# Optimization experiments

Hardware: AMD Instinct MI355X
Metric: run time of the kernel (lower is better)

The kernel has to match this reference:

```python
import jax, jax.numpy as jnp
import numpy as np

H = 16          # n_heads
HID = 64        # QASS MLP hidden dim


def setup_inputs() -> dict:
    key = jax.random.key(0)
    ks = jax.random.split(key, 12)
    B, N, D = 2, 2048, 1024
    Dh = D // H
    inp = {
        "query": jax.random.normal(ks[0], (B, N, D), jnp.float32),
        "key": jax.random.normal(ks[1], (B, N, D), jnp.float32),
        "value": jax.random.normal(ks[2], (B, N, D), jnp.float32),
        "allowed_mask": jnp.ones((1, 1, N, N), dtype=bool),
        # projection weights, torch Linear convention: y = x @ W.T, W: [out, in]
        "wq": jax.random.normal(ks[3], (D, D), jnp.float32) * (D ** -0.5),
        "wk": jax.random.normal(ks[4], (D, D), jnp.float32) * (D ** -0.5),
        "wv": jax.random.normal(ks[5], (D, D), jnp.float32) * (D ** -0.5),
        "wo": jax.random.normal(ks[6], (D, D), jnp.float32) * (D ** -0.5),
        # QASS scaler weights
        "wb1": jax.random.normal(ks[7], (HID, 1), jnp.float32),          # mlp_base[0]
        "wb2": jax.random.normal(ks[8], (H * Dh, HID), jnp.float32) * (HID ** -0.5),  # mlp_base[2]
        "wg1": jax.random.normal(ks[9], (HID, Dh), jnp.float32) * (Dh ** -0.5),       # mlp_gate[0]
        "wg2": jax.random.normal(ks[10], (Dh, HID), jnp.float32) * (HID ** -0.5),     # mlp_gate[2]
        "n_context": 2048,
    }
    return inp


def _gelu(x):
    return jax.nn.gelu(x, approximate=False)  # torch nn.GELU default (erf)


def reference(query, key, value, allowed_mask, wq, wk, wv, wo, wb1, wb2, wg1, wg2, n_context):
    B, N, D = query.shape
    Dh = D // H

    def split_heads(x):  # [B,N,D] -> [B,H,N,Dh]
        return x.reshape(B, N, H, Dh).transpose(0, 2, 1, 3)

    q = split_heads(query @ wq.T)
    k = split_heads(key @ wk.T)
    v = split_heads(value @ wv.T)

    # QASS scaling: q * base(log n) * (1 + tanh(gate(q)))   (n_context > 1)
    log_n = jnp.log(jnp.asarray(n_context, jnp.float32))
    base = (_gelu(log_n * wb1[:, 0]) @ wb2.T).reshape(1, H, 1, Dh)  # [1,H,1,Dh]
    gate = 1.0 + jnp.tanh(_gelu(q @ wg1.T) @ wg2.T)                  # [B,H,N,Dh]
    q = q * base * gate

    scores = jnp.einsum("bhnd,bhmd->bhnm", q, k) / jnp.sqrt(jnp.float32(Dh))
    scores = jnp.where(allowed_mask, scores, -jnp.inf)
    attn = jax.nn.softmax(scores, axis=-1)  # dropout p=0 -> identity
    out = jnp.einsum("bhnm,bhmd->bhnd", attn, v)
    out = out.transpose(0, 2, 1, 3).reshape(B, N, D)
    return out @ wo.T
```

## Files before the change

kernel.cpp:

```cpp
#include <hip/hip_runtime.h>
#include <math.h>


typedef _Float16 half_t;
using half8   = __attribute__((ext_vector_type(8))) _Float16;
using bhalf8  = __attribute__((ext_vector_type(8))) short;
using floatx4 = __attribute__((ext_vector_type(4))) float;

__device__ inline unsigned short f2bf(float f) {
  union { float f; unsigned int u; } v; v.f = f;
  unsigned int u = v.u;
  u = u + 0x7fffu + ((u >> 16) & 1u);
  return (unsigned short)(u >> 16);
}
__device__ inline float bf2f(unsigned short h) {
  union { unsigned int u; float f; } v; v.u = ((unsigned int)h) << 16;
  return v.f;
}
__device__ inline float gelu_f(float x) {
  return 0.5f * x * (1.0f + erff(x * 0.70710678118654752440f));
}
__device__ __forceinline__ unsigned int cvtpk_bf16(float lo, float hi) {
  unsigned int r;
  asm("v_cvt_pk_bf16_f32 %0, %1, %2" : "=v"(r) : "v"(lo), "v"(hi));
  return r;
}

#define MFMAF16(a, b, c)  __builtin_amdgcn_mfma_f32_16x16x32_f16((a), (b), (c), 0, 0, 0)
#define MFMABF16(a, b, c) __builtin_amdgcn_mfma_f32_16x16x32_bf16((a), (b), (c), 0, 0, 0)

__device__ __forceinline__ void dma16(const void* g, void* l) {
  __builtin_amdgcn_global_load_lds(
      (const __attribute__((address_space(1))) unsigned int*)g,
      (__attribute__((address_space(3))) unsigned int*)l, 16, 0, 0);
}

__global__ __launch_bounds__(256) void k_cvtbase(
    const float* __restrict__ q, const float* __restrict__ k, const float* __restrict__ v,
    const float* __restrict__ wq, const float* __restrict__ wk,
    const float* __restrict__ wv, const float* __restrict__ wo,
    half_t* __restrict__ q16, half_t* __restrict__ k16, half_t* __restrict__ v16,
    half_t* __restrict__ w16,
    const float* __restrict__ wb1, const float* __restrict__ wb2,
    const int* __restrict__ nctx, float* __restrict__ base_out) {
  int tid = threadIdx.x;
  if (blockIdx.x >= 8192) {
    __shared__ float h1[64];
    float logn = logf((float)(*nctx));
    if (tid < 64) h1[tid] = gelu_f(logn * wb1[tid]);
    __syncthreads();
    int i = (blockIdx.x - 8192) * 256 + tid;
    float s = 0.f;
#pragma unroll
    for (int j = 0; j < 64; j++) s += h1[j] * wb2[i * 64 + j];
    base_out[i] = s;
    return;
  }
  size_t e = ((size_t)blockIdx.x * 256 + tid) * 8;
  const float* src; half_t* dst; size_t off;
  if (e < (size_t)3 * 4194304) {
    int t = (int)(e >> 22); off = e & 4194303;
    src = (t == 0) ? q : (t == 1 ? k : v);
    dst = (t == 0) ? q16 : (t == 1 ? k16 : v16);
  } else {
    size_t e2 = e - (size_t)3 * 4194304;
    int t = (int)(e2 >> 20); off = (e2 & 1048575);
    src = (t == 0) ? wq : (t == 1 ? wk : (t == 2 ? wv : wo));
    dst = w16 + (size_t)t * 1048576;
  }
  float4 a = *(const float4*)(src + off);
  float4 b = *(const float4*)(src + off + 4);
  half8 h;
  h[0] = (half_t)a.x; h[1] = (half_t)a.y; h[2] = (half_t)a.z; h[3] = (half_t)a.w;
  h[4] = (half_t)b.x; h[5] = (half_t)b.y; h[6] = (half_t)b.z; h[7] = (half_t)b.w;
  *(half8*)(dst + off) = h;
}

template <int MODE>
__global__ __launch_bounds__(256, 3) void k_gemm(const half_t* __restrict__ Abase,
                                                 const half_t* __restrict__ Wbase,
                                                 half_t* __restrict__ qp16,
                                                 half_t* __restrict__ kswz,
                                                 unsigned short* __restrict__ vtl,
                                                 float* __restrict__ outf) {
  const int z = (MODE == 0) ? blockIdx.z : 0;
  const half_t* Ag = Abase + (size_t)z * 4194304;
  const half_t* Wg = Wbase + (size_t)z * 1048576;
  __shared__ __align__(16) half_t SM[4][128 * 32];
  const int tid = threadIdx.x, lane = tid & 63, w = tid >> 6;
  const int quad = lane >> 4, lm = lane & 15;
  const int wm = w >> 1, wn = w & 1;
  const int bm0 = blockIdx.y * 128, bn0 = blockIdx.x * 128;

  const floatx4 zero4 = {0.f, 0.f, 0.f, 0.f};
  floatx4 acc[4][4];
#pragma unroll
  for (int i = 0; i < 4; i++)
#pragma unroll
    for (int j = 0; j < 4; j++) acc[i][j] = zero4;

  const int j4 = lane >> 2;
  const int cs = (lane & 3) ^ (((j4 & 3) + (j4 >> 2)) & 3);
  const int ub = ((lm & 3) + (lm >> 2)) & 3;

#pragma unroll
  for (int i = 0; i < 2; i++) {
    int tr = w * 32 + i * 16 + j4;
    dma16((const char*)Ag + ((size_t)(bm0 + tr) * 1024 + cs * 8) * 2,
          (char*)SM[0] + (w * 32 + i * 16) * 64);
    dma16((const char*)Wg + ((size_t)(bn0 + tr) * 1024 + cs * 8) * 2,
          (char*)SM[2] + (w * 32 + i * 16) * 64);
  }

  for (int kk = 0; kk < 1024; kk += 32) {
    const int cur = (kk >> 5) & 1;
    __syncthreads();
    if (kk < 992) {
#pragma unroll
      for (int i = 0; i < 2; i++) {
        int tr = w * 32 + i * 16 + j4;
        dma16((const char*)Ag + ((size_t)(bm0 + tr) * 1024 + kk + 32 + cs * 8) * 2,
              (char*)SM[cur ^ 1] + (w * 32 + i * 16) * 64);
        dma16((const char*)Wg + ((size_t)(bn0 + tr) * 1024 + kk + 32 + cs * 8) * 2,
              (char*)SM[2 + (cur ^ 1)] + (w * 32 + i * 16) * 64);
      }
    }

    const half_t* as_ = SM[cur];
    const half_t* bs_ = SM[2 + cur];
    half8 af[4], bf[4];
#pragma unroll
    for (int tm = 0; tm < 4; tm++)
      af[tm] = *(const half8*)&as_[(wm * 64 + tm * 16 + lm) * 32
                                   + ((quad ^ ub) << 3)];
#pragma unroll
    for (int tn = 0; tn < 4; tn++)
      bf[tn] = *(const half8*)&bs_[(wn * 64 + tn * 16 + lm) * 32
                                   + ((quad ^ ub) << 3)];
#pragma unroll
    for (int tm = 0; tm < 4; tm++)
#pragma unroll
      for (int tn = 0; tn < 4; tn++)
        acc[tm][tn] = MFMAF16(af[tm], bf[tn], acc[tm][tn]);
  }

  if constexpr (MODE == 3) {
#pragma unroll
    for (int tm = 0; tm < 4; tm++)
#pragma unroll
      for (int tn = 0; tn < 4; tn++)
#pragma unroll
        for (int rr = 0; rr < 4; rr++) {
          int gm = bm0 + wm * 64 + tm * 16 + quad * 4 + rr;
          int gn = bn0 + wn * 64 + tn * 16 + lm;
          outf[(size_t)gm * 1024 + gn] = acc[tm][tn][rr];
        }
  } else if (z == 0) {
#pragma unroll
    for (int tm = 0; tm < 4; tm++)
#pragma unroll
      for (int tn = 0; tn < 4; tn++)
#pragma unroll
        for (int rr = 0; rr < 4; rr++) {
          int gm = bm0 + wm * 64 + tm * 16 + quad * 4 + rr;
          int gn = bn0 + wn * 64 + tn * 16 + lm;
          int b = gm >> 11, n = gm & 2047, hd = gn >> 6, d = gn & 63;
          qp16[((size_t)((b << 4) + hd) * 2048 + n) * 64 + d] = (half_t)acc[tm][tn][rr];
        }
  } else if (z == 1) {
    half_t* smh = (half_t*)&SM[0][0];
    __syncthreads();
#pragma unroll
    for (int tm = 0; tm < 4; tm++)
#pragma unroll
      for (int tn = 0; tn < 4; tn++) {
        int gnl = wn * 64 + tn * 16 + lm;
        int hl = gnl >> 6, d = gnl & 63;
#pragma unroll
        for (int rr = 0; rr < 4; rr++) {
          int nl = wm * 64 + tm * 16 + quad * 4 + rr;
          int sw = ((((d >> 3) ^ (nl & 7)) << 3) | (d & 7));
          smh[(hl * 128 + nl) * 64 + sw] = (half_t)acc[tm][tn][rr];
        }
      }
    __syncthreads();
    {
      const int b = bm0 >> 11, n0 = bm0 & 2047, hd0 = bn0 >> 6;
#pragma unroll
      for (int c = 0; c < 8; c++) {
        int lin = (c * 256 + tid) * 8;
        int hl = lin >> 13, nl = (lin >> 6) & 127, j0 = lin & 63;
        size_t row = (size_t)((b << 4) + hd0 + hl) * 2048 + n0 + nl;
        *(half8*)(kswz + row * 64 + j0) = *(const half8*)(smh + lin);
      }
    }
  } else {
    unsigned short* sm = (unsigned short*)&SM[0][0];
    __syncthreads();
#pragma unroll
    for (int tm = 0; tm < 4; tm++) {
      int nlb = wm * 64 + tm * 16 + quad * 4;
      int tl = (nlb >> 6) & 1, nnb = nlb & 63;
      int kc4 = nnb >> 5;
      int qd = (nnb >> 2) & 3;
      int jb = (nnb >> 4) & 1;
#pragma unroll
      for (int tn = 0; tn < 4; tn++) {
        int gnl = wn * 64 + tn * 16 + lm;
        int hl = gnl >> 6, d = gnl & 63;
        int inner0 = (qd * 16 + (d & 15)) * 32 + (d >> 4) * 8 + jb * 4;
        unsigned int u0 = __float_as_uint(acc[tm][tn][0]) + 0x8000u;
        unsigned int u1 = __float_as_uint(acc[tm][tn][1]) + 0x8000u;
        unsigned int u2 = __float_as_uint(acc[tm][tn][2]) + 0x8000u;
        unsigned int u3 = __float_as_uint(acc[tm][tn][3]) + 0x8000u;
        uint2 pk;
        pk.x = __builtin_amdgcn_perm(u1, u0, 0x07060302u);
        pk.y = __builtin_amdgcn_perm(u3, u2, 0x07060302u);
        *(uint2*)&sm[(((hl * 2 + tl) * 2 + kc4) * 2048) + inner0] = pk;
      }
    }
    __syncthreads();
    {
      const int b = bm0 >> 11, t0 = (bm0 & 2047) >> 6, hd0 = bn0 >> 6;
#pragma unroll
      for (int c = 0; c < 8; c++) {
        int lin = (c * 256 + tid) * 8;
        int page = lin >> 11;
        int hl = page >> 2, tl = (page >> 1) & 1, kc4 = page & 1;
        int inner = lin & 2047;
        size_t idx = ((size_t)(((b << 4) + hd0 + hl) * 32 + t0 + tl) * 2 + kc4) * 2048
                   + (size_t)inner;
        *(bhalf8*)(vtl + idx) = *(const bhalf8*)(sm + lin);
      }
    }
  }
}

__global__ __launch_bounds__(256) void k_gate(const half_t* __restrict__ qp,
                                              const float* __restrict__ base_v,
                                              const float* __restrict__ wg1,
                                              const float* __restrict__ wg2,
                                              half_t* __restrict__ qs) {
  __shared__ __align__(16) half_t W1[64 * 72];
  __shared__ __align__(16) half_t W2[64 * 72];
  __shared__ __align__(16) half_t HT[4][16 * 72];
  const int tid = threadIdx.x, lane = tid & 63, w = tid >> 6;
  const int quad = lane >> 4, lm = lane & 15;
  for (int i = tid; i < 4096; i += 256) {
    int j = i >> 6, d = i & 63;
    W1[j * 72 + d] = (half_t)wg1[i];
    W2[j * 72 + d] = (half_t)wg2[i];
  }
  __syncthreads();
  const int R0 = blockIdx.x * 256;
  const int hd = (R0 >> 11) & 15;
  float bsev[4];
#pragma unroll
  for (int tn = 0; tn < 4; tn++) bsev[tn] = base_v[hd * 64 + tn * 16 + lm];
  const float cs = 0.18033688011112042f;
  const floatx4 zero4 = {0.f, 0.f, 0.f, 0.f};
  half_t* ht = HT[w];

  for (int ti = 0; ti < 4; ti++) {
    int r0 = R0 + w * 64 + ti * 16;
    half8 aq0 = *(const half8*)&qp[(size_t)(r0 + lm) * 64 + quad * 8];
    half8 aq1 = *(const half8*)&qp[(size_t)(r0 + lm) * 64 + 32 + quad * 8];
    floatx4 hc[4];
#pragma unroll
    for (int tn = 0; tn < 4; tn++) {
      half8 b0 = *(const half8*)&W1[(tn * 16 + lm) * 72 + quad * 8];
      half8 b1 = *(const half8*)&W1[(tn * 16 + lm) * 72 + 32 + quad * 8];
      floatx4 t = zero4;
      t = MFMAF16(aq0, b0, t);
      t = MFMAF16(aq1, b1, t);
      hc[tn] = t;
    }
#pragma unroll
    for (int tn = 0; tn < 4; tn++)
#pragma unroll
      for (int rr = 0; rr < 4; rr++)
        ht[(quad * 4 + rr) * 72 + tn * 16 + lm] = (half_t)gelu_f(hc[tn][rr]);
    half8 ah0 = *(const half8*)&ht[lm * 72 + quad * 8];
    half8 ah1 = *(const half8*)&ht[lm * 72 + 32 + quad * 8];
#pragma unroll
    for (int tn = 0; tn < 4; tn++) {
      half8 b0 = *(const half8*)&W2[(tn * 16 + lm) * 72 + quad * 8];
      half8 b1 = *(const half8*)&W2[(tn * 16 + lm) * 72 + 32 + quad * 8];
      floatx4 t = zero4;
      t = MFMAF16(ah0, b0, t);
      t = MFMAF16(ah1, b1, t);
#pragma unroll
      for (int rr = 0; rr < 4; rr++) {
        int row = r0 + quad * 4 + rr;
        int d = tn * 16 + lm;
        float qv = (float)qp[(size_t)row * 64 + d];
        float g = 1.0f + tanhf(t[rr]);
        qs[(size_t)row * 64 + d] = (half_t)(qv * bsev[tn] * g * cs);
      }
    }
  }
}

__global__ __launch_bounds__(256, 2) void k_attn(const half_t* __restrict__ qs,
                                                 const half_t* __restrict__ kswz,
                                                 const unsigned short* __restrict__ vtl,
                                                 unsigned short* __restrict__ Opart,
                                                 float* __restrict__ rpart) {
  __shared__ __align__(16) half_t KH[2][64 * 64];

  const int tid = threadIdx.x;
  const int lane = tid & 63;
  const int w = tid >> 6;
  const int quad = lane >> 4;
  const int lm = lane & 15;
  const int a7 = lm & 7;
  const int hd = blockIdx.x;
  const int qg = blockIdx.y >> 1, half = blockIdx.y & 1;
  const int b = blockIdx.z;
  const int bh = b * 16 + hd;
  const size_t hb = (size_t)bh * 2048 * 64;
  const char* khT = (const char*)(kswz + hb);
  const unsigned short* vtT = vtl + (size_t)bh * 32 * 4096;

  half8 qh[4][2];
#pragma unroll
  for (int rg = 0; rg < 4; rg++)
#pragma unroll
    for (int kc = 0; kc < 2; kc++)
      qh[rg][kc] = *(const half8*)(qs + hb
          + (size_t)(qg * 256 + w * 64 + rg * 16 + lm) * 64 + kc * 32 + quad * 8);

  const floatx4 zero4 = {0.f, 0.f, 0.f, 0.f};
  floatx4 O[4][4];
#pragma unroll
  for (int rg = 0; rg < 4; rg++)
#pragma unroll
    for (int dt = 0; dt < 4; dt++) O[rg][dt] = zero4;
  floatx4 racc[4];
#pragma unroll
  for (int rg = 0; rg < 4; rg++) racc[rg] = zero4;
  const short one_bf = (short)0x3F80;
  const bhalf8 vones = {one_bf, one_bf, one_bf, one_bf,
                        one_bf, one_bf, one_bf, one_bf};

  const int lo16 = lane * 16;
  const size_t g0 = (size_t)half * 16 * 8192;

#pragma unroll
  for (int r = 0; r < 2; r++) {
    int sb = (w * 2 + r) * 1024;
    dma16(khT + g0 + sb + lo16, (char*)KH[0] + sb);
  }

  for (int t = 0; t < 16; t++) {
    const int cur = t & 1;
    __syncthreads();

    const unsigned short* vb = vtT + ((size_t)(half * 16 + t) * 2) * 2048 + lane * 32;
    bhalf8 vf[2][4];
#pragma unroll
    for (int kc4 = 0; kc4 < 2; kc4++)
#pragma unroll
      for (int dt = 0; dt < 4; dt++)
        vf[kc4][dt] = *(const bhalf8*)(vb + kc4 * 2048 + dt * 8);

    if (t < 15) {
      const size_t gof = g0 + (size_t)(t + 1) * 8192;
#pragma unroll
      for (int r = 0; r < 2; r++) {
        int sb = (w * 2 + r) * 1024;
        dma16(khT + gof + sb + lo16, (char*)KH[cur ^ 1] + sb);
      }
    }

    const half_t* kh_ = KH[cur];

#pragma unroll
    for (int p = 0; p < 2; p++) {
      floatx4 s[2][4];
#pragma unroll
      for (int ri = 0; ri < 2; ri++)
#pragma unroll
        for (int kb = 0; kb < 4; kb++) s[ri][kb] = zero4;

      __builtin_amdgcn_s_setprio(1);
#pragma unroll
      for (int kb = 0; kb < 4; kb++)
#pragma unroll
        for (int kc = 0; kc < 2; kc++) {
          int addr = (kb * 16 + lm) * 64 + (((kc * 4 + quad) ^ a7) << 3);
          half8 khf = *(const half8*)&kh_[addr];
#pragma unroll
          for (int ri = 0; ri < 2; ri++)
            s[ri][kb] = MFMAF16(khf, qh[p * 2 + ri][kc], s[ri][kb]);
        }
      __builtin_amdgcn_s_setprio(0);

#pragma unroll
      for (int ri = 0; ri < 2; ri++) {
        const int rg = p * 2 + ri;
        float e[4][4];
#pragma unroll
        for (int kb = 0; kb < 4; kb++)
#pragma unroll
          for (int rr = 0; rr < 4; rr++)
            e[kb][rr] = __builtin_amdgcn_exp2f(s[ri][kb][rr]);

        __builtin_amdgcn_s_setprio(1);
#pragma unroll
        for (int kc4 = 0; kc4 < 2; kc4++) {
          union { unsigned int w4[4]; bhalf8 v; } pa;
          pa.w4[0] = cvtpk_bf16(e[2 * kc4][0],     e[2 * kc4][1]);
          pa.w4[1] = cvtpk_bf16(e[2 * kc4][2],     e[2 * kc4][3]);
          pa.w4[2] = cvtpk_bf16(e[2 * kc4 + 1][0], e[2 * kc4 + 1][1]);
          pa.w4[3] = cvtpk_bf16(e[2 * kc4 + 1][2], e[2 * kc4 + 1][3]);
          racc[rg] = MFMABF16(pa.v, vones, racc[rg]);
#pragma unroll
          for (int dt = 0; dt < 4; dt++)
            O[rg][dt] = MFMABF16(pa.v, vf[kc4][dt], O[rg][dt]);
        }
        __builtin_amdgcn_s_setprio(0);
      }
    }
  }

  unsigned short* op = Opart + (size_t)half * 65536 * 64;
  float* rp = rpart + (size_t)half * 65536;
#pragma unroll
  for (int rg = 0; rg < 4; rg++) {
#pragma unroll
    for (int rr = 0; rr < 4; rr++) {
      int n = qg * 256 + w * 64 + rg * 16 + quad * 4 + rr;
      size_t row = (size_t)bh * 2048 + n;
      if (lm == 0) rp[row] = racc[rg][rr];
#pragma unroll
      for (int dt = 0; dt < 4; dt++)
        op[row * 64 + dt * 16 + lm] = f2bf(O[rg][dt][rr]);
    }
  }
}

__global__ __launch_bounds__(256) void k_combine(const unsigned short* __restrict__ Opart,
                                                 const float* __restrict__ rpart,
                                                 half_t* __restrict__ obf) {
  size_t e = ((size_t)blockIdx.x * 256 + threadIdx.x) * 8;
  size_t row = e >> 6; int d0 = (int)(e & 63);
  float inv = 1.0f / (rpart[row] + rpart[65536 + row]);
  bhalf8 o0 = *(const bhalf8*)&Opart[row * 64 + d0];
  bhalf8 o1 = *(const bhalf8*)&Opart[(size_t)65536 * 64 + row * 64 + d0];
  int b = (int)(row >> 15), h = (int)((row >> 11) & 15), n = (int)(row & 2047);
  half8 o;
#pragma unroll
  for (int j = 0; j < 8; j++)
    o[j] = (half_t)((bf2f((unsigned short)o0[j]) + bf2f((unsigned short)o1[j])) * inv);
  *(half8*)&obf[((size_t)(b * 2048 + n)) * 1024 + h * 64 + d0] = o;
}

extern "C" void kernel_launch(void* const* d_in, const int* in_sizes, int n_in,
                              void* d_out, int out_size, void* d_ws, size_t ws_size,
                              hipStream_t stream) {
  const float* query = (const float*)d_in[0];
  const float* key_  = (const float*)d_in[1];
  const float* value = (const float*)d_in[2];
  const float* wq  = (const float*)d_in[4];
  const float* wk  = (const float*)d_in[5];
  const float* wv  = (const float*)d_in[6];
  const float* wo  = (const float*)d_in[7];
  const float* wb1 = (const float*)d_in[8];
  const float* wb2 = (const float*)d_in[9];
  const float* wg1 = (const float*)d_in[10];
  const float* wg2 = (const float*)d_in[11];
  const int* nctx  = (const int*)d_in[12];
  float* out = (float*)d_out;

  char* ws = (char*)d_ws;
  size_t o = 0;
  float* base_v = (float*)(ws + o); o += 4096;
  half_t* q16   = (half_t*)(ws + o); o += (size_t)4096 * 1024 * 2;
  half_t* k16   = (half_t*)(ws + o); o += (size_t)4096 * 1024 * 2;
  half_t* v16   = (half_t*)(ws + o); o += (size_t)4096 * 1024 * 2;
  half_t* w16   = (half_t*)(ws + o); o += (size_t)4 * 1024 * 1024 * 2;
  half_t* qp16  = (half_t*)(ws + o); o += (size_t)4096 * 1024 * 2;
  half_t* kswz  = (half_t*)(ws + o); o += (size_t)4096 * 1024 * 2;
  unsigned short* vtl = (unsigned short*)(ws + o); o += (size_t)4096 * 1024 * 2;
  unsigned short* Opart = (unsigned short*)(ws + o); o += (size_t)2 * 65536 * 64 * 2;
  float* rpart = (float*)(ws + o); o += (size_t)2 * 65536 * 4;
  half_t* qs  = q16;
  half_t* obf = k16;

  k_cvtbase<<<8196, 256, 0, stream>>>(query, key_, value, wq, wk, wv, wo,
                                      q16, k16, v16, w16, wb1, wb2, nctx, base_v);
  k_gemm<0><<<dim3(8, 32, 3), 256, 0, stream>>>(q16, w16, qp16, kswz, vtl, nullptr);
  k_gate<<<256, 256, 0, stream>>>(qp16, base_v, wg1, wg2, qs);
  k_attn<<<dim3(16, 16, 2), 256, 0, stream>>>(qs, kswz, vtl, Opart, rpart);
  k_combine<<<2048, 256, 0, stream>>>(Opart, rpart, obf);
  k_gemm<3><<<dim3(8, 32, 1), 256, 0, stream>>>(obf, w16 + (size_t)3 * 1048576,
                                                nullptr, nullptr, nullptr, out);
}
```

Before: 250.5 us.

## Load K tiles directly from global into registers, dropping LDS staging and barriers

The attention kernel no longer DMAs swizzled K tiles into shared memory with double buffering and a barrier each iteration. Each lane now reads its K fragments straight from global memory into registers, ping-ponging between two register sets, and the loop is unrolled by two so the next tile's load overlaps the current tile's compute. This removes the LDS traffic and __syncthreads, but each wave now fetches K itself, which adds redundant global/L2 reads and register pressure that may hurt occupancy under launch_bounds(256,2).

```diff
diff --git a/kernel.cpp b/kernel.cpp
--- a/kernel.cpp
+++ b/kernel.cpp
@@ -306,8 +306,6 @@
                                                  const unsigned short* __restrict__ vtl,
                                                  unsigned short* __restrict__ Opart,
                                                  float* __restrict__ rpart) {
-  __shared__ __align__(16) half_t KH[2][64 * 64];
-
   const int tid = threadIdx.x;
   const int lane = tid & 63;
   const int w = tid >> 6;
@@ -319,7 +317,7 @@
   const int b = blockIdx.z;
   const int bh = b * 16 + hd;
   const size_t hb = (size_t)bh * 2048 * 64;
-  const char* khT = (const char*)(kswz + hb);
+  const char* khT = (const char*)(kswz + hb) + (size_t)half * 16 * 8192;
   const unsigned short* vtT = vtl + (size_t)bh * 32 * 4096;
 
   half8 qh[4][2];
@@ -343,86 +341,93 @@
   const bhalf8 vones = {one_bf, one_bf, one_bf, one_bf,
                         one_bf, one_bf, one_bf, one_bf};
 
-  const int lo16 = lane * 16;
-  const size_t g0 = (size_t)half * 16 * 8192;
-
-#pragma unroll
-  for (int r = 0; r < 2; r++) {
-    int sb = (w * 2 + r) * 1024;
-    dma16(khT + g0 + sb + lo16, (char*)KH[0] + sb);
-  }
-
-  for (int t = 0; t < 16; t++) {
-    const int cur = t & 1;
-    __syncthreads();
-
-    const unsigned short* vb = vtT + ((size_t)(half * 16 + t) * 2) * 2048 + lane * 32;
+  int koff[4][2];
+#pragma unroll
+  for (int kb = 0; kb < 4; kb++)
+#pragma unroll
+    for (int kc = 0; kc < 2; kc++)
+      koff[kb][kc] = ((kb * 16 + lm) * 64 + (((kc * 4 + quad) ^ a7) << 3)) * 2;
+
+#define LOADK(DST, T)                                                          \
+  _Pragma("unroll")                                                            \
+  for (int kb = 0; kb < 4; kb++)                                               \
+    _Pragma("unroll")                                                          \
+    for (int kc = 0; kc < 2; kc++)                                             \
+      DST[kb * 2 + kc] =                                                       \
+          *(const half8*)(khT + (size_t)(T) * 8192 + koff[kb][kc]);
+
+#define LOADV(DST, T)                                                          \
+  {                                                                            \
+    const unsigned short* vb =                                                 \
+        vtT + ((size_t)(half * 16 + (T)) * 2) * 2048 + lane * 32;              \
+    _Pragma("unroll")                                                          \
+    for (int kc4 = 0; kc4 < 2; kc4++)                                          \
+      _Pragma("unroll")                                                        \
+      for (int dt = 0; dt < 4; dt++)                                           \
+        DST[kc4][dt] = *(const bhalf8*)(vb + kc4 * 2048 + dt * 8);             \
+  }
+
+#define TILE_COMPUTE(KF, VF)                                                   \
+  {                                                                            \
+    _Pragma("unroll")                                                          \
+    for (int p = 0; p < 2; p++) {                                              \
+      floatx4 s[2][4];                                                         \
+      _Pragma("unroll")                                                        \
+      for (int ri = 0; ri < 2; ri++)                                           \
+        _Pragma("unroll")                                                      \
+        for (int kb = 0; kb < 4; kb++) s[ri][kb] = zero4;                      \
+      __builtin_amdgcn_s_setprio(1);                                           \
+      _Pragma("unroll")                                                        \
+      for (int kb = 0; kb < 4; kb++)                                           \
+        _Pragma("unroll")                                                      \
+        for (int kc = 0; kc < 2; kc++) {                                       \
+          half8 khf = KF[kb * 2 + kc];                                         \
+          _Pragma("unroll")                                                    \
+          for (int ri = 0; ri < 2; ri++)                                       \
+            s[ri][kb] = MFMAF16(khf, qh[p * 2 + ri][kc], s[ri][kb]);           \
+        }                                                                      \
+      __builtin_amdgcn_s_setprio(0);                                           \
+      _Pragma("unroll")                                                        \
+      for (int ri = 0; ri < 2; ri++) {                                         \
+        const int rg = p * 2 + ri;                                             \
+        float e[4][4];                                                         \
+        _Pragma("unroll")                                                      \
+        for (int kb = 0; kb < 4; kb++)                                         \
+          _Pragma("unroll")                                                    \
+          for (int rr = 0; rr < 4; rr++)                                       \
+            e[kb][rr] = __builtin_amdgcn_exp2f(s[ri][kb][rr]);                 \
+        __builtin_amdgcn_s_setprio(1);                                         \
+        _Pragma("unroll")                                                      \
+        for (int kc4 = 0; kc4 < 2; kc4++) {                                    \
+          union { unsigned int w4[4]; bhalf8 v; } pa;                          \
+          pa.w4[0] = cvtpk_bf16(e[2 * kc4][0],     e[2 * kc4][1]);             \
+          pa.w4[1] = cvtpk_bf16(e[2 * kc4][2],     e[2 * kc4][3]);             \
+          pa.w4[2] = cvtpk_bf16(e[2 * kc4 + 1][0], e[2 * kc4 + 1][1]);         \
+          pa.w4[3] = cvtpk_bf16(e[2 * kc4 + 1][2], e[2 * kc4 + 1][3]);         \
+          racc[rg] = MFMABF16(pa.v, vones, racc[rg]);                          \
+          _Pragma("unroll")                                                    \
+          for (int dt = 0; dt < 4; dt++)                                       \
+            O[rg][dt] = MFMABF16(pa.v, VF[kc4][dt], O[rg][dt]);                \
+        }                                                                      \
+        __builtin_amdgcn_s_setprio(0);                                         \
+      }                                                                        \
+    }                                                                          \
+  }
+
+  half8 kfA[8], kfB[8];
+  LOADK(kfA, 0);
+  for (int t = 0; t < 16; t += 2) {
     bhalf8 vf[2][4];
-#pragma unroll
-    for (int kc4 = 0; kc4 < 2; kc4++)
-#pragma unroll
-      for (int dt = 0; dt < 4; dt++)
-        vf[kc4][dt] = *(const bhalf8*)(vb + kc4 * 2048 + dt * 8);
-
-    if (t < 15) {
-      const size_t gof = g0 + (size_t)(t + 1) * 8192;
-#pragma unroll
-      for (int r = 0; r < 2; r++) {
-        int sb = (w * 2 + r) * 1024;
-        dma16(khT + gof + sb + lo16, (char*)KH[cur ^ 1] + sb);
-      }
-    }
-
-    const half_t* kh_ = KH[cur];
-
-#pragma unroll
-    for (int p = 0; p < 2; p++) {
-      floatx4 s[2][4];
-#pragma unroll
-      for (int ri = 0; ri < 2; ri++)
-#pragma unroll
-        for (int kb = 0; kb < 4; kb++) s[ri][kb] = zero4;
-
-      __builtin_amdgcn_s_setprio(1);
-#pragma unroll
-      for (int kb = 0; kb < 4; kb++)
-#pragma unroll
-        for (int kc = 0; kc < 2; kc++) {
-          int addr = (kb * 16 + lm) * 64 + (((kc * 4 + quad) ^ a7) << 3);
-          half8 khf = *(const half8*)&kh_[addr];
-#pragma unroll
-          for (int ri = 0; ri < 2; ri++)
-            s[ri][kb] = MFMAF16(khf, qh[p * 2 + ri][kc], s[ri][kb]);
-        }
-      __builtin_amdgcn_s_setprio(0);
-
-#pragma unroll
-      for (int ri = 0; ri < 2; ri++) {
-        const int rg = p * 2 + ri;
-        float e[4][4];
-#pragma unroll
-        for (int kb = 0; kb < 4; kb++)
-#pragma unroll
-          for (int rr = 0; rr < 4; rr++)
-            e[kb][rr] = __builtin_amdgcn_exp2f(s[ri][kb][rr]);
-
-        __builtin_amdgcn_s_setprio(1);
-#pragma unroll
-        for (int kc4 = 0; kc4 < 2; kc4++) {
-          union { unsigned int w4[4]; bhalf8 v; } pa;
-          pa.w4[0] = cvtpk_bf16(e[2 * kc4][0],     e[2 * kc4][1]);
-          pa.w4[1] = cvtpk_bf16(e[2 * kc4][2],     e[2 * kc4][3]);
-          pa.w4[2] = cvtpk_bf16(e[2 * kc4 + 1][0], e[2 * kc4 + 1][1]);
-          pa.w4[3] = cvtpk_bf16(e[2 * kc4 + 1][2], e[2 * kc4 + 1][3]);
-          racc[rg] = MFMABF16(pa.v, vones, racc[rg]);
-#pragma unroll
-          for (int dt = 0; dt < 4; dt++)
-            O[rg][dt] = MFMABF16(pa.v, vf[kc4][dt], O[rg][dt]);
-        }
-        __builtin_amdgcn_s_setprio(0);
-      }
-    }
-  }
+    LOADV(vf, t);
+    LOADK(kfB, t + 1);
+    TILE_COMPUTE(kfA, vf);
+    LOADV(vf, t + 1);
+    if (t < 14) LOADK(kfA, t + 2);
+    TILE_COMPUTE(kfB, vf);
+  }
+#undef LOADK
+#undef LOADV
+#undef TILE_COMPUTE
 
   unsigned short* op = Opart + (size_t)half * 65536 * 64;
   float* rp = rpart + (size_t)half * 65536;
```

After: 319.6 us. 27.6% more time.
